# Performance work log

Hardware: AMD Instinct MI355X
Metric: run time of the kernel (lower is better)

## Reference

```python
import jax, jax.numpy as jnp
import numpy as np

N = 8192          # rays
S = 128           # steps per ray (cfg.n_steps_fixed)
POS_BANDS = 10    # positional-encoding bands for positions
VD_BANDS = 4      # bands for view directions (default in _encode_viewdir)
EARLY_STOP_T = 1e-4


def pos_enc(x, num_bands):
    """[..., 3] -> [..., 3 + 2*3*num_bands], interleaved [x, sin(f*x), cos(f*x), ...]."""
    parts = [x]
    for i in range(num_bands):  # small fixed loop over frequency bands
        f = jnp.asarray(2.0 ** i, dtype=x.dtype)
        parts.append(jnp.sin(f * x))
        parts.append(jnp.cos(f * x))
    return jnp.concatenate(parts, axis=-1)


def setup_inputs() -> dict:
    key = jax.random.key(0)
    ks = jax.random.split(key, 10)
    orig = 0.1 * jax.random.normal(ks[0], (N, 3), jnp.float32)
    dirs = jax.random.normal(ks[1], (N, 3), jnp.float32)
    dirs = dirs / (jnp.linalg.norm(dirs, axis=-1, keepdims=True) + 1e-8)
    tmin = 0.5 + 0.5 * jax.random.uniform(ks[2], (N,), jnp.float32)
    tmax = tmin + 1.0 + jax.random.uniform(ks[3], (N,), jnp.float32)
    d_enc = 3 + 2 * 3 * POS_BANDS          # 63
    d_vd = 3 + 2 * 3 * VD_BANDS            # 27
    hid, feat = 64, 15
    W1 = jax.random.normal(ks[4], (d_enc, hid), jnp.float32) / np.sqrt(d_enc)
    b1 = jnp.zeros((hid,), jnp.float32)
    W2 = jax.random.normal(ks[5], (hid, 1 + feat), jnp.float32) / np.sqrt(hid)
    b2 = jnp.zeros((1 + feat,), jnp.float32)
    V1 = jax.random.normal(ks[6], (feat + d_vd, hid), jnp.float32) / np.sqrt(feat + d_vd)
    c1 = jnp.zeros((hid,), jnp.float32)
    V2 = jax.random.normal(ks[7], (hid, 3), jnp.float32) / np.sqrt(hid)
    c2 = jnp.zeros((3,), jnp.float32)
    return {"orig": orig, "dirs": dirs, "tmin": tmin, "tmax": tmax,
            "W1": W1, "b1": b1, "W2": W2, "b2": b2,
            "V1": V1, "c1": c1, "V2": V2, "c2": c2}


def reference(orig, dirs, tmin, tmax, W1, b1, W2, b2, V1, c1, V2, c2):
    # --- fixed-step sampling ---
    t_uniform = jnp.linspace(0.0, 1.0, S, dtype=jnp.float32)          # [S]
    t = tmin[:, None] + t_uniform[None, :] * (tmax - tmin)[:, None]   # [N, S]
    dt = jnp.mean(tmax - tmin) / S                                    # scalar step size

    # --- positions and encoder ---
    pos = orig[:, None, :] + dirs[:, None, :] * t[..., None]          # [N, S, 3]
    enc = pos_enc(pos, POS_BANDS)                                     # [N, S, 63]

    # --- field MLP: sigma + rgb features ---
    h = jax.nn.relu(enc @ W1 + b1)                                    # [N, S, 64]
    out = h @ W2 + b2                                                 # [N, S, 16]
    sigma = jax.nn.relu(out[..., 0])                                  # [N, S]
    rgb_feat = out[..., 1:]                                           # [N, S, 15]

    # --- rgb head with view-direction PE ---
    vd = dirs / (jnp.linalg.norm(dirs, axis=-1, keepdims=True) + 1e-8)
    vd_enc = pos_enc(vd, VD_BANDS)                                    # [N, 27]
    vd_enc = jnp.broadcast_to(vd_enc[:, None, :], (rgb_feat.shape[0], S, vd_enc.shape[-1]))
    rgb_in = jnp.concatenate([rgb_feat, vd_enc], axis=-1)             # [N, S, 42]
    rgb_steps = jax.nn.sigmoid(jax.nn.relu(rgb_in @ V1 + c1) @ V2 + c2)  # [N, S, 3]

    # --- alpha compositing with early stop (dense-masked equivalent) ---
    alpha = 1.0 - jnp.exp(-sigma * dt)                                # [N, S]
    one_minus = 1.0 - alpha
    T_excl = jnp.concatenate(
        [jnp.ones_like(alpha[:, :1]), jnp.cumprod(one_minus, axis=1)[:, :-1]], axis=1
    )                                                                 # transmittance before each step
    active = T_excl > EARLY_STOP_T                                    # ray still marching
    weights = T_excl * alpha * active                                 # [N, S]
    rgb_out = jnp.sum(weights[..., None] * rgb_steps, axis=1)         # [N, 3]
    T_out = jnp.prod(jnp.where(active, one_minus, 1.0), axis=1)       # final transmittance at stop
    return rgb_out, T_out
```

## Files before the change

### kernel.cpp

```cpp
#include <hip/hip_runtime.h>
#include <hip/hip_bf16.h>

#define NRAYS 8192
#define SAMP  128
#define DVD   27
#define NFEAT 15

typedef float  f32x4  __attribute__((ext_vector_type(4)));
typedef short  short8 __attribute__((ext_vector_type(8)));
typedef unsigned int u32x2 __attribute__((ext_vector_type(2)));
typedef unsigned int u32x4 __attribute__((ext_vector_type(4)));

#define GVC_OFF  16896
#define IMG_CHUNKS 1056

static __device__ __forceinline__ int XB(int row, int cb) {
    return row * 128 + (cb ^ ((row & 7) << 4));
}
static __device__ __forceinline__ int XS(int row, int k) {
    return row * 64 + (k ^ ((row & 7) << 3));
}

static __device__ __forceinline__ void stbf(short* p, float x) {
    union { unsigned u; struct { short lo, hi; } s; } v;
    v.u = __float_as_uint(x) + 0x8000u;
    *p = v.s.hi;
}
static __device__ __forceinline__ float bf2f(short s) {
    return __uint_as_float(((unsigned)(unsigned short)s) << 16);
}
static __device__ __forceinline__ unsigned pk2bf(float lo, float hi) {
    unsigned r;
    asm("v_cvt_pk_bf16_f32 %0, %1, %2" : "=v"(r) : "v"(lo), "v"(hi));
    return r;
}
static __device__ __forceinline__ float sin_fast(float x) {
    float r = x * 0.15915494309189535f;
    r = r - floorf(r);
    return __builtin_amdgcn_sinf(r);
}
static __device__ __forceinline__ float cos_fast(float x) {
    float r = x * 0.15915494309189535f;
    r = r - floorf(r);
    return __builtin_amdgcn_cosf(r);
}
static __device__ __forceinline__ float sigm(float x) {
    return 1.0f / (1.0f + __expf(-x));
}

static __device__ __forceinline__ int kmap(int r) {
    if (r == 0) return 30;
    if (r == 1) return 31;
    if (r == 2) return 62;
    const int q = r - 3, i = q / 6, c = q - 6 * i;
    return (i < 5 ? 6 * i : 32 + 6 * (i - 5)) + c;
}

__global__ void __launch_bounds__(256)
prep_kernel(const float* __restrict__ W1, const float* __restrict__ b1,
            const float* __restrict__ W2, const float* __restrict__ b2,
            const float* __restrict__ V1, const float* __restrict__ c1,
            const float* __restrict__ V2, const float* __restrict__ tmin,
            const float* __restrict__ tmax, short* __restrict__ img,
            float* __restrict__ gvc) {
    if (blockIdx.x == 34) {
        __shared__ float red[4];
        const int tid = threadIdx.x, lane = tid & 63, wave = tid >> 6;
        const float4* tm0 = (const float4*)tmin;
        const float4* tm1 = (const float4*)tmax;
        float s = 0.0f;
        #pragma unroll
        for (int it = 0; it < 8; it++) {
            const int i = tid + it * 256;
            const float4 a = tm1[i], b = tm0[i];
            s += (a.x - b.x) + (a.y - b.y) + (a.z - b.z) + (a.w - b.w);
        }
        #pragma unroll
        for (int off = 32; off > 0; off >>= 1)
            s += __shfl_xor(s, off, 64);
        if (lane == 0) red[wave] = s;
        __syncthreads();
        if (tid == 0)
            gvc[64] = (red[0] + red[1] + red[2] + red[3]) *
                      (1.0f / ((float)NRAYS * (float)SAMP));
        return;
    }
    const int g = blockIdx.x * 256 + threadIdx.x;
    if (g < 4032) {
        const int r = g >> 6, n = g & 63;
        const int prow = (n & 3) * 16 + (n >> 2);
        stbf(&img[XS(prow, kmap(r))], W1[g]);
    } else if (g < 4096) {
        const int n = g - 4032;
        const int prow = (n & 3) * 16 + (n >> 2);
        stbf(&img[XS(prow, 63)], b1[n]);
    } else if (g < 8192) {
        const int i = g - 4096;
        const int k = i >> 6, n = i & 63;
        const int prow = (n & 3) * 16 + (n >> 2);
        float a = 0.0f;
        #pragma unroll
        for (int j = 0; j < 15; j++) a += W2[k * 16 + 1 + j] * V1[j * 64 + n];
        stbf(&img[4096 + XS(prow, k)], a);
    } else if (g < 8256) {
        const int k = g - 8192;
        stbf(&img[8192 + k], W2[k * 16]);
    } else if (g < 8448) {
        const int i = g - 8256, c = i >> 6, k = i & 63;
        stbf(&img[8192 + 64 + c * 64 + k], V2[k * 3 + c]);
    } else if (g < 8512) {
        const int n = g - 8448;
        float a = c1[n];
        #pragma unroll
        for (int j = 0; j < 15; j++) a += b2[1 + j] * V1[j * 64 + n];
        gvc[n] = a;
    }
}

#define SMEM_BYTES 38400

__global__ void __launch_bounds__(256, 4)
march_kernel(const float* __restrict__ orig,
             const float* __restrict__ dirs,
             const float* __restrict__ tmin,
             const float* __restrict__ tmax,
             const float* __restrict__ b2,
             const float* __restrict__ c2,
             const float* __restrict__ V1,
             const short* __restrict__ img,
             const float* __restrict__ gvc,
             float* __restrict__ out) {
    __shared__ __align__(16) char smem[SMEM_BYTES];
    char*  const sEc   = smem;
    char*  const sW1tc = smem + 16384;
    char*  const sCtc  = smem + 24576;
    short* const sSm   = (short*)(smem + 32768);
    float* const sOm   = (float*)(smem + 33280);
    short* const sRgb  = (short*)(smem + 35328);
    float* const sVde  = (float*)(smem);

    const int tid  = threadIdx.x;
    const int lane = tid & 63;
    const int wave = tid >> 6;
    const int ray  = blockIdx.x * 4 + wave;

    {
        const u32x4* src = (const u32x4*)img;
        u32x4* dst = (u32x4*)(smem + 16384);
        #pragma unroll
        for (int it = 0; it < 5; it++) {
            const int i = tid + it * 256;
            if (i < IMG_CHUNKS) dst[i] = src[i];
        }
    }

    const float ox = orig[ray * 3 + 0];
    const float oy = orig[ray * 3 + 1];
    const float oz = orig[ray * 3 + 2];
    const float dx = dirs[ray * 3 + 0];
    const float dy = dirs[ray * 3 + 1];
    const float dz = dirs[ray * 3 + 2];
    const float t0v = tmin[ray];
    const float trange = tmax[ray] - t0v;
    const float negdtv = -gvc[64];

    {
        const float nrm = sqrtf(dx * dx + dy * dy + dz * dz);
        const float inv = 1.0f / (nrm + 1e-8f);
        const float vx = dx * inv, vy = dy * inv, vz = dz * inv;
        if (lane < DVD) {
            float val;
            if (lane < 3) {
                val = (lane == 0) ? vx : ((lane == 1) ? vy : vz);
            } else {
                const int q = lane - 3;
                const int b = q / 6;
                const int r = q - 6 * b;
                const bool isSin = (r < 3);
                const int d = isSin ? r : (r - 3);
                const float comp = (d == 0) ? vx : ((d == 1) ? vy : vz);
                const float a = (float)(1 << b) * comp;
                val = isSin ? sin_fast(a) : cos_fast(a);
            }
            sVde[wave * 28 + lane] = val;
        }
    }
    __syncthreads();

    const int nfr  = lane & 15;
    const int quad = lane >> 4;
    const int cbq  = quad * 16;

    float gv[4];
    {
        const f32x4 g0 = *(const f32x4*)&gvc[4 * nfr];
        gv[0] = g0.x; gv[1] = g0.y; gv[2] = g0.z; gv[3] = g0.w;
    }
    #pragma unroll 9
    for (int q = 0; q < DVD; q++) {
        const float e = sVde[wave * 28 + q];
        const f32x4 vv = *(const f32x4*)&V1[(NFEAT + q) * 64 + 4 * nfr];
        gv[0] += e * vv.x; gv[1] += e * vv.y;
        gv[2] += e * vv.z; gv[3] += e * vv.w;
    }

    const float bb2 = b2[0];
    const float bc2 = (nfr < 3) ? c2[nfr] : 0.0f;

    __syncthreads();

    char* const myE = sEc + wave * 4096;

    const int sl   = lane >> 1;
    const int half = lane & 1;
    const float fmul = half ? 5.0929581789406507f
                            : 0.15915494309189535f;

    const float dt32 = (32.0f / 127.0f) * trange;
    const float pdx = dx * dt32, pdy = dy * dt32, pdz = dz * dt32;
    const float tseed = t0v + (float)sl * ((1.0f / 127.0f) * trange);
    float px = ox + dx * tseed, py = oy + dy * tseed, pz = oz + dz * tseed;
    float sx, cx, sy, cy, sz, cz;
    {
        float r;
        r = px * fmul; r -= floorf(r);
        sx = __builtin_amdgcn_sinf(r); cx = __builtin_amdgcn_cosf(r);
        r = py * fmul; r -= floorf(r);
        sy = __builtin_amdgcn_sinf(r); cy = __builtin_amdgcn_cosf(r);
        r = pz * fmul; r -= floorf(r);
        sz = __builtin_amdgcn_sinf(r); cz = __builtin_amdgcn_cosf(r);
    }
    float sDx, cDx, sDy, cDy, sDz, cDz;
    {
        float r;
        r = pdx * fmul; r -= floorf(r);
        sDx = __builtin_amdgcn_sinf(r); cDx = __builtin_amdgcn_cosf(r);
        r = pdy * fmul; r -= floorf(r);
        sDy = __builtin_amdgcn_sinf(r); cDy = __builtin_amdgcn_cosf(r);
        r = pdz * fmul; r -= floorf(r);
        sDz = __builtin_amdgcn_sinf(r); cDz = __builtin_amdgcn_cosf(r);
    }

    #pragma unroll 1
    for (int qq = 0; qq < 4; qq++) {
        {
            float wsx = sx, wcx = cx, wsy = sy, wcy = cy, wsz = sz, wcz = cz;
            unsigned e[16] __attribute__((aligned(16)));
            #pragma unroll
            for (int j = 0; j < 5; j++) {
                e[3 * j + 0] = pk2bf(wsx, wsy);
                e[3 * j + 1] = pk2bf(wsz, wcx);
                e[3 * j + 2] = pk2bf(wcy, wcz);
                if (j < 4) {
                    const float tx = wsx + wsx, ty = wsy + wsy, tz = wsz + wsz;
                    const float nsx = tx * wcx, nsy = ty * wcy, nsz = tz * wcz;
                    wcx = __builtin_fmaf(-tx, wsx, 1.0f);
                    wcy = __builtin_fmaf(-ty, wsy, 1.0f);
                    wcz = __builtin_fmaf(-tz, wsz, 1.0f);
                    wsx = nsx; wsy = nsy; wsz = nsz;
                }
            }
            e[15] = half ? pk2bf(pz, 1.0f) : pk2bf(px, py);
            #pragma unroll
            for (int w = 0; w < 4; w++)
                *(u32x4*)(myE + XB(sl, half * 64 + w * 16)) =
                    *(const u32x4*)&e[4 * w];
        }
        {
            const float nsx = __builtin_fmaf(sx, cDx, cx * sDx);
            cx = __builtin_fmaf(cx, cDx, -(sx * sDx)); sx = nsx;
            const float nsy = __builtin_fmaf(sy, cDy, cy * sDy);
            cy = __builtin_fmaf(cy, cDy, -(sy * sDy)); sy = nsy;
            const float nsz = __builtin_fmaf(sz, cDz, cz * sDz);
            cz = __builtin_fmaf(cz, cDz, -(sz * sDz)); sz = nsz;
            px += pdx; py += pdy; pz += pdz;
        }
        f32x4 acc1[2][4];
        {
            short8 af[2][2];
            #pragma unroll
            for (int mt = 0; mt < 2; mt++)
                #pragma unroll
                for (int kt = 0; kt < 2; kt++)
                    af[mt][kt] = *(const short8*)(myE + XB(nfr + 16 * mt, cbq + kt * 64));
            __builtin_amdgcn_s_setprio(1);
            #pragma unroll
            for (int nt = 0; nt < 4; nt++) {
                const short8 wf0 = *(const short8*)
                    (sW1tc + XB(nt * 16 + nfr, cbq));
                #pragma unroll
                for (int mt = 0; mt < 2; mt++)
                    acc1[mt][nt] = __builtin_amdgcn_mfma_f32_16x16x32_bf16(
                        af[mt][0], wf0, (f32x4){0.0f, 0.0f, 0.0f, 0.0f}, 0, 0, 0);
                const short8 wf1 = *(const short8*)
                    (sW1tc + XB(nt * 16 + nfr, cbq + 64));
                #pragma unroll
                for (int mt = 0; mt < 2; mt++)
                    acc1[mt][nt] = __builtin_amdgcn_mfma_f32_16x16x32_bf16(
                        af[mt][1], wf1, acc1[mt][nt], 0, 0, 0);
            }
            __builtin_amdgcn_s_setprio(0);
        }
        #pragma unroll
        for (int mt = 0; mt < 2; mt++)
            #pragma unroll
            for (int r = 0; r < 4; r++) {
                const int m = 4 * quad + r + 16 * mt;
                u32x2 hp;
                hp.x = pk2bf(fmaxf(acc1[mt][0][r], 0.0f),
                             fmaxf(acc1[mt][1][r], 0.0f));
                hp.y = pk2bf(fmaxf(acc1[mt][2][r], 0.0f),
                             fmaxf(acc1[mt][3][r], 0.0f));
                *(u32x2*)(myE + XB(m, 8 * nfr)) = hp;
            }
        short8 ah[2][2];
        #pragma unroll
        for (int mt = 0; mt < 2; mt++)
            #pragma unroll
            for (int kt = 0; kt < 2; kt++)
                ah[mt][kt] = *(const short8*)(myE + XB(nfr + 16 * mt, cbq + kt * 64));
        {
            f32x4 acc2[2];
            acc2[0] = (f32x4){bb2, bb2, bb2, bb2};
            acc2[1] = (f32x4){bb2, bb2, bb2, bb2};
            short8 w2sf[2];
            #pragma unroll
            for (int kt = 0; kt < 2; kt++)
                w2sf[kt] = *(const short8*)&sSm[quad * 8 + kt * 32];
            __builtin_amdgcn_s_setprio(1);
            #pragma unroll
            for (int mt = 0; mt < 2; mt++)
                #pragma unroll
                for (int kt = 0; kt < 2; kt++)
                    acc2[mt] = __builtin_amdgcn_mfma_f32_16x16x32_bf16(
                        ah[mt][kt], w2sf[kt], acc2[mt], 0, 0, 0);
            __builtin_amdgcn_s_setprio(0);
            if (nfr == 0) {
                #pragma unroll
                for (int mt = 0; mt < 2; mt++)
                    #pragma unroll
                    for (int r = 0; r < 4; r++) {
                        const int m = 4 * quad + r + 16 * mt;
                        sOm[wave * 128 + qq * 32 + m] =
                            fmaxf(acc2[mt][r], 0.0f) * negdtv;
                    }
            }
        }
        #pragma unroll
        for (int nth = 0; nth < 2; nth++) {
            f32x4 acc3[2][2];
            #pragma unroll
            for (int mt = 0; mt < 2; mt++)
                #pragma unroll
                for (int j = 0; j < 2; j++) {
                    const float gvi = gv[2 * nth + j];
                    acc3[mt][j] = (f32x4){gvi, gvi, gvi, gvi};
                }
            __builtin_amdgcn_s_setprio(1);
            #pragma unroll
            for (int j = 0; j < 2; j++)
                #pragma unroll
                for (int kt = 0; kt < 2; kt++) {
                    const short8 cf = *(const short8*)
                        (sCtc + XB((2 * nth + j) * 16 + nfr, cbq + kt * 64));
                    #pragma unroll
                    for (int mt = 0; mt < 2; mt++)
                        acc3[mt][j] = __builtin_amdgcn_mfma_f32_16x16x32_bf16(
                            ah[mt][kt], cf, acc3[mt][j], 0, 0, 0);
                }
            __builtin_amdgcn_s_setprio(0);
            #pragma unroll
            for (int mt = 0; mt < 2; mt++)
                #pragma unroll
                for (int r = 0; r < 4; r++) {
                    const int m = 4 * quad + r + 16 * mt;
                    *(unsigned*)(myE + XB(m, 8 * nfr + 4 * nth)) =
                        pk2bf(fmaxf(acc3[mt][0][r], 0.0f),
                              fmaxf(acc3[mt][1][r], 0.0f));
                }
        }
        {
            f32x4 acc4[2];
            acc4[0] = (f32x4){bc2, bc2, bc2, bc2};
            acc4[1] = (f32x4){bc2, bc2, bc2, bc2};
            short8 agg[2][2];
            #pragma unroll
            for (int mt = 0; mt < 2; mt++)
                #pragma unroll
                for (int kt = 0; kt < 2; kt++)
                    agg[mt][kt] = *(const short8*)(myE + XB(nfr + 16 * mt, cbq + kt * 64));
            const int vr = 1 + ((nfr < 3) ? nfr : 2);
            short8 v2f[2];
            #pragma unroll
            for (int kt = 0; kt < 2; kt++)
                v2f[kt] = *(const short8*)&sSm[vr * 64 + quad * 8 + kt * 32];
            __builtin_amdgcn_s_setprio(1);
            #pragma unroll
            for (int mt = 0; mt < 2; mt++)
                #pragma unroll
                for (int kt = 0; kt < 2; kt++)
                    acc4[mt] = __builtin_amdgcn_mfma_f32_16x16x32_bf16(
                        agg[mt][kt], v2f[kt], acc4[mt], 0, 0, 0);
            __builtin_amdgcn_s_setprio(0);
            if (nfr < 3) {
                #pragma unroll
                for (int mt = 0; mt < 2; mt++)
                    #pragma unroll
                    for (int r = 0; r < 4; r++) {
                        const int m = 4 * quad + r + 16 * mt;
                        stbf(&sRgb[wave * 384 + (qq * 32 + m) * 3 + nfr],
                             acc4[mt][r]);
                    }
            }
        }
    }

    const float om0 = __expf(sOm[wave * 128 + 2 * lane]);
    const float om1 = __expf(sOm[wave * 128 + 2 * lane + 1]);
    const float al0 = 1.0f - om0;
    const float al1 = 1.0f - om1;

    float inc = om0 * om1;
    #pragma unroll
    for (int off = 1; off < 64; off <<= 1) {
        const float q = __shfl_up(inc, off, 64);
        if (lane >= off) inc *= q;
    }
    float Texc = __shfl_up(inc, 1, 64);
    if (lane == 0) Texc = 1.0f;

    const float T0 = Texc;
    const float T1 = Texc * om0;
    const float a0 = (T0 > 1e-4f) ? 1.0f : 0.0f;
    const float a1 = (T1 > 1e-4f) ? 1.0f : 0.0f;
    const float w0 = T0 * al0 * a0;
    const float w1 = T1 * al1 * a1;

    float cr = w0 * sigm(bf2f(sRgb[wave * 384 + (2 * lane) * 3 + 0])) +
               w1 * sigm(bf2f(sRgb[wave * 384 + (2 * lane + 1) * 3 + 0]));
    float cg = w0 * sigm(bf2f(sRgb[wave * 384 + (2 * lane) * 3 + 1])) +
               w1 * sigm(bf2f(sRgb[wave * 384 + (2 * lane + 1) * 3 + 1]));
    float cb = w0 * sigm(bf2f(sRgb[wave * 384 + (2 * lane) * 3 + 2])) +
               w1 * sigm(bf2f(sRgb[wave * 384 + (2 * lane + 1) * 3 + 2]));
    float tp = (a0 > 0.0f ? om0 : 1.0f) * (a1 > 0.0f ? om1 : 1.0f);

    #pragma unroll
    for (int off = 32; off > 0; off >>= 1) {
        cr += __shfl_xor(cr, off, 64);
        cg += __shfl_xor(cg, off, 64);
        cb += __shfl_xor(cb, off, 64);
        tp *= __shfl_xor(tp, off, 64);
    }

    if (lane == 0) {
        out[ray * 3 + 0] = cr;
        out[ray * 3 + 1] = cg;
        out[ray * 3 + 2] = cb;
        out[NRAYS * 3 + ray] = tp;
    }
}

extern "C" void kernel_launch(void* const* d_in, const int* in_sizes, int n_in,
                              void* d_out, int out_size, void* d_ws, size_t ws_size,
                              hipStream_t stream) {
    const float* orig = (const float*)d_in[0];
    const float* dirs = (const float*)d_in[1];
    const float* tmin = (const float*)d_in[2];
    const float* tmax = (const float*)d_in[3];
    const float* W1   = (const float*)d_in[4];
    const float* b1   = (const float*)d_in[5];
    const float* W2   = (const float*)d_in[6];
    const float* b2   = (const float*)d_in[7];
    const float* V1   = (const float*)d_in[8];
    const float* c1   = (const float*)d_in[9];
    const float* V2   = (const float*)d_in[10];
    const float* c2   = (const float*)d_in[11];

    short* img = (short*)d_ws;
    float* gvc = (float*)((char*)d_ws + GVC_OFF);

    prep_kernel<<<35, 256, 0, stream>>>(W1, b1, W2, b2, V1, c1, V2,
                                        tmin, tmax, img, gvc);
    march_kernel<<<NRAYS / 4, 256, 0, stream>>>(orig, dirs, tmin, tmax,
                                                b2, c2, V1, img, gvc,
                                                (float*)d_out);
}
```

Measured before the change: 114.3 us.

## Software-pipeline final RGB MFMA stage across iterations and widen hidden-layer stores

Defers the last RGB layer (V2 MFMA and rgb store) of each 32-sample chunk into the next loop iteration, after the next chunk's encoding has been written. The hidden activations are preloaded into registers at the end of each iteration and the last chunk is drained after the loop. The goal is to overlap the LDS read latency and the dependent MFMA chain with independent work. It also merges the two half-passes of the V1 layer into one pass with 4 accumulator tiles per M-tile, so each row's hidden activations go out as one 64-bit LDS store. This raises register pressure and drops the setprio hints around the deferred MFMAs.

After: 113.2 us. No clear change (-1.0%).

```diff
diff --git a/kernel.cpp b/kernel.cpp
--- a/kernel.cpp
+++ b/kernel.cpp
@@ -241,6 +241,34 @@
         sDz = __builtin_amdgcn_sinf(r); cDz = __builtin_amdgcn_cosf(r);
     }
 
+    short8 agg[2][2];
+    auto v2_block = [&](int qv) {
+        f32x4 acc4[2];
+        acc4[0] = (f32x4){bc2, bc2, bc2, bc2};
+        acc4[1] = (f32x4){bc2, bc2, bc2, bc2};
+        const int vr = 1 + ((nfr < 3) ? nfr : 2);
+        short8 v2f[2];
+        #pragma unroll
+        for (int kt = 0; kt < 2; kt++)
+            v2f[kt] = *(const short8*)&sSm[vr * 64 + quad * 8 + kt * 32];
+        #pragma unroll
+        for (int mt = 0; mt < 2; mt++)
+            #pragma unroll
+            for (int kt = 0; kt < 2; kt++)
+                acc4[mt] = __builtin_amdgcn_mfma_f32_16x16x32_bf16(
+                    agg[mt][kt], v2f[kt], acc4[mt], 0, 0, 0);
+        if (nfr < 3) {
+            #pragma unroll
+            for (int mt = 0; mt < 2; mt++)
+                #pragma unroll
+                for (int r = 0; r < 4; r++) {
+                    const int m = 4 * quad + r + 16 * mt;
+                    stbf(&sRgb[wave * 384 + (qv * 32 + m) * 3 + nfr],
+                         acc4[mt][r]);
+                }
+        }
+    };
+
     #pragma unroll 1
     for (int qq = 0; qq < 4; qq++) {
         {
@@ -275,6 +303,7 @@
             cz = __builtin_fmaf(cz, cDz, -(sz * sDz)); sz = nsz;
             px += pdx; py += pdy; pz += pdz;
         }
+        if (qq > 0) v2_block(qq - 1);
         f32x4 acc1[2][4];
         {
             short8 af[2][2];
@@ -346,27 +375,24 @@
                     }
             }
         }
-        #pragma unroll
-        for (int nth = 0; nth < 2; nth++) {
-            f32x4 acc3[2][2];
+        {
+            f32x4 acc3[2][4];
             #pragma unroll
             for (int mt = 0; mt < 2; mt++)
                 #pragma unroll
-                for (int j = 0; j < 2; j++) {
-                    const float gvi = gv[2 * nth + j];
-                    acc3[mt][j] = (f32x4){gvi, gvi, gvi, gvi};
-                }
+                for (int nt = 0; nt < 4; nt++)
+                    acc3[mt][nt] = (f32x4){gv[nt], gv[nt], gv[nt], gv[nt]};
             __builtin_amdgcn_s_setprio(1);
             #pragma unroll
-            for (int j = 0; j < 2; j++)
+            for (int nt = 0; nt < 4; nt++)
                 #pragma unroll
                 for (int kt = 0; kt < 2; kt++) {
                     const short8 cf = *(const short8*)
-                        (sCtc + XB((2 * nth + j) * 16 + nfr, cbq + kt * 64));
+                        (sCtc + XB(nt * 16 + nfr, cbq + kt * 64));
                     #pragma unroll
                     for (int mt = 0; mt < 2; mt++)
-                        acc3[mt][j] = __builtin_amdgcn_mfma_f32_16x16x32_bf16(
-                            ah[mt][kt], cf, acc3[mt][j], 0, 0, 0);
+                        acc3[mt][nt] = __builtin_amdgcn_mfma_f32_16x16x32_bf16(
+                            ah[mt][kt], cf, acc3[mt][nt], 0, 0, 0);
                 }
             __builtin_amdgcn_s_setprio(0);
             #pragma unroll
@@ -374,46 +400,21 @@
                 #pragma unroll
                 for (int r = 0; r < 4; r++) {
                     const int m = 4 * quad + r + 16 * mt;
-                    *(unsigned*)(myE + XB(m, 8 * nfr + 4 * nth)) =
-                        pk2bf(fmaxf(acc3[mt][0][r], 0.0f),
-                              fmaxf(acc3[mt][1][r], 0.0f));
+                    u32x2 gp;
+                    gp.x = pk2bf(fmaxf(acc3[mt][0][r], 0.0f),
+                                 fmaxf(acc3[mt][1][r], 0.0f));
+                    gp.y = pk2bf(fmaxf(acc3[mt][2][r], 0.0f),
+                                 fmaxf(acc3[mt][3][r], 0.0f));
+                    *(u32x2*)(myE + XB(m, 8 * nfr)) = gp;
                 }
         }
-        {
-            f32x4 acc4[2];
-            acc4[0] = (f32x4){bc2, bc2, bc2, bc2};
-            acc4[1] = (f32x4){bc2, bc2, bc2, bc2};
-            short8 agg[2][2];
-            #pragma unroll
-            for (int mt = 0; mt < 2; mt++)
-                #pragma unroll
-                for (int kt = 0; kt < 2; kt++)
-                    agg[mt][kt] = *(const short8*)(myE + XB(nfr + 16 * mt, cbq + kt * 64));
-            const int vr = 1 + ((nfr < 3) ? nfr : 2);
-            short8 v2f[2];
+        #pragma unroll
+        for (int mt = 0; mt < 2; mt++)
             #pragma unroll
             for (int kt = 0; kt < 2; kt++)
-                v2f[kt] = *(const short8*)&sSm[vr * 64 + quad * 8 + kt * 32];
-            __builtin_amdgcn_s_setprio(1);
-            #pragma unroll
-            for (int mt = 0; mt < 2; mt++)
-                #pragma unroll
-                for (int kt = 0; kt < 2; kt++)
-                    acc4[mt] = __builtin_amdgcn_mfma_f32_16x16x32_bf16(
-                        agg[mt][kt], v2f[kt], acc4[mt], 0, 0, 0);
-            __builtin_amdgcn_s_setprio(0);
-            if (nfr < 3) {
-                #pragma unroll
-                for (int mt = 0; mt < 2; mt++)
-                    #pragma unroll
-                    for (int r = 0; r < 4; r++) {
-                        const int m = 4 * quad + r + 16 * mt;
-                        stbf(&sRgb[wave * 384 + (qq * 32 + m) * 3 + nfr],
-                             acc4[mt][r]);
-                    }
-            }
-        }
-    }
+                agg[mt][kt] = *(const short8*)(myE + XB(nfr + 16 * mt, cbq + kt * 64));
+    }
+    v2_block(3);
 
     const float om0 = __expf(sOm[wave * 128 + 2 * lane]);
     const float om1 = __expf(sOm[wave * 128 + 2 * lane + 1]);
```
